# Kernel optimization log

Measured on AMD Instinct MI355X. Metric: run time of the kernel, lower is better.

Reference implementation:

```python
import jax, jax.numpy as jnp
import numpy as np

NUM_EMBEDDINGS = 1024
EMBEDDING_DIM = 256
COMMITMENT_COST = 0.25


def setup_inputs() -> dict:
    key = jax.random.key(0)
    k1, k2 = jax.random.split(key)
    z = jax.random.normal(k1, (64, EMBEDDING_DIM, 32, 32), dtype=jnp.float32)
    # torch init: uniform(-1/K, 1/K)
    emb = jax.random.uniform(k2, (NUM_EMBEDDINGS, EMBEDDING_DIM), dtype=jnp.float32,
                             minval=-1.0 / NUM_EMBEDDINGS, maxval=1.0 / NUM_EMBEDDINGS)
    return {"z": z, "emb": emb}


def reference(z, emb):
    B, D, H, W = z.shape
    # [B, H, W, D] -> [N, D]
    z_flat = jnp.transpose(z, (0, 2, 3, 1)).reshape(-1, D)
    # squared-euclidean distances to codebook: [N, K]
    d = ((z_flat * z_flat).sum(axis=1, keepdims=True)
         + (emb * emb).sum(axis=1)
         - 2.0 * z_flat @ emb.T)
    indices = jnp.argmin(d, axis=1)                      # [N]
    z_q = emb[indices].reshape(B, H, W, D).transpose(0, 3, 1, 2)  # [B, D, H, W]

    codebook_loss = jnp.mean((z_q - jax.lax.stop_gradient(z)) ** 2)
    commitment_loss = jnp.mean((z - jax.lax.stop_gradient(z_q)) ** 2)
    loss = codebook_loss + COMMITMENT_COST * commitment_loss

    # straight-through estimator
    z_q_out = z + jax.lax.stop_gradient(z_q - z)
    return z_q_out, loss, indices.reshape(B, H, W)
```

## Files before the change

### kernel.cpp

```cpp
#include <hip/hip_runtime.h>


typedef _Float16 f16x8 __attribute__((ext_vector_type(8)));
typedef float f32x4 __attribute__((ext_vector_type(4)));

#define VQ_W 1.5e-3f
#define SCR_LDS_BYTES 35328
#define RES_LDS_BYTES 33792

__device__ __forceinline__ float sq_rnd(float v) {
  float y = v * v;
  asm volatile("" : "+v"(y));
  return y;
}

__device__ float np_pw256_sq(const float* base, int stride) {
  float tot0, tot1;
  {
    const float* a = base;
    float r[8];
    #pragma unroll
    for (int j = 0; j < 8; ++j) r[j] = sq_rnd(a[j * stride]);
    #pragma unroll 1
    for (int i = 8; i < 128; i += 8) {
      #pragma unroll
      for (int j = 0; j < 8; ++j) r[j] += sq_rnd(a[(i + j) * stride]);
    }
    tot0 = ((r[0] + r[1]) + (r[2] + r[3])) + ((r[4] + r[5]) + (r[6] + r[7]));
  }
  {
    const float* a = base + 128 * stride;
    float r[8];
    #pragma unroll
    for (int j = 0; j < 8; ++j) r[j] = sq_rnd(a[j * stride]);
    #pragma unroll 1
    for (int i = 8; i < 128; i += 8) {
      #pragma unroll
      for (int j = 0; j < 8; ++j) r[j] += sq_rnd(a[(i + j) * stride]);
    }
    tot1 = ((r[0] + r[1]) + (r[2] + r[3])) + ((r[4] + r[5]) + (r[6] + r[7]));
  }
  return tot0 + tot1;
}

__global__ __launch_bounds__(256) void vq_pre(const float* __restrict__ emb,
                                              const float* __restrict__ z,
                                              _Float16* __restrict__ Ef,
                                              float* __restrict__ embT,
                                              float* __restrict__ e2,
                                              float* __restrict__ z2) {
  __shared__ float sm[256];
  const int tid = threadIdx.x;
  if (blockIdx.x < 1024) {
    const int g = blockIdx.x * 256 + tid;
    const float v = emb[g];
    Ef[g] = (_Float16)v;
    const int k = g >> 8, d = g & 255;
    embT[d * 1024 + k] = v;
    if (g < 1024) e2[g] = np_pw256_sq(emb + g * 256, 1);
    return;
  }
  const int blk = blockIdx.x - 1024;
  const int p = tid & 15;
  const int c = tid >> 4;
  const int n0 = blk * 16;
  const int n = n0 + p;
  const int bb = n >> 10, hw = n & 1023;
  const float* zp = z + bb * 262144 + hw;
  const int dbase = (c >> 3) * 128 + (c & 7);
  float r = sq_rnd(zp[dbase * 1024]);
  #pragma unroll
  for (int i = 1; i < 16; ++i) r += sq_rnd(zp[(dbase + 8 * i) * 1024]);
  sm[c * 16 + p] = r;
  __syncthreads();
  if (tid < 16) {
    const int pp = tid;
    float h0[8], h1[8];
    #pragma unroll
    for (int j = 0; j < 8; ++j) {
      h0[j] = sm[j * 16 + pp];
      h1[j] = sm[(8 + j) * 16 + pp];
    }
    const float tot0 = ((h0[0] + h0[1]) + (h0[2] + h0[3])) +
                       ((h0[4] + h0[5]) + (h0[6] + h0[7]));
    const float tot1 = ((h1[0] + h1[1]) + (h1[2] + h1[3])) +
                       ((h1[4] + h1[5]) + (h1[6] + h1[7]));
    z2[n0 + pp] = tot0 + tot1;
  }
}

__global__ __launch_bounds__(256, 4) void vq_screen(
    const float* __restrict__ z, const _Float16* __restrict__ Ef,
    const float* __restrict__ e2, const float* __restrict__ z2,
    int* __restrict__ gcnt, unsigned short* __restrict__ gcand) {
  extern __shared__ __align__(16) char smem[];
  unsigned* runminU = (unsigned*)(smem + 32768);
  int* cnt = (int*)(smem + 33024);
  unsigned short* cand = (unsigned short*)(smem + 33280);

  const int tid = threadIdx.x;
  const int blk = blockIdx.x;
  const int n0 = blk * 64;
  const int bb = blk >> 4;
  const int hw0 = (blk & 15) * 64;
  const float* zb = z + bb * 262144 + hw0;

  if (tid < 64) { runminU[tid] = 0x7F800000u; cnt[tid] = 0; }

  {
    const int p = tid & 63, dh = tid >> 6;
    #pragma unroll
    for (int dq = 0; dq < 8; ++dq) {
      const int d0 = dh * 64 + dq * 8;
      f16x8 hv;
      #pragma unroll
      for (int j = 0; j < 8; ++j) hv[j] = (_Float16)zb[(d0 + j) * 1024 + p];
      *(f16x8*)&smem[p * 512 + ((d0 * 2) ^ ((p & 7) * 16))] = hv;
    }
  }

  const int l = tid & 63;
  const int ln = l & 15;
  const int q = l >> 4;
  const int wc = tid >> 6;
  const int xr = (l & 7) * 16;

  float z2r[4][4];
  #pragma unroll
  for (int fi = 0; fi < 4; ++fi)
    #pragma unroll
    for (int rg = 0; rg < 4; ++rg)
      z2r[fi][rg] = z2[n0 + fi * 16 + q * 4 + rg];

  f32x4 acc[4][4];
  #pragma unroll
  for (int fi = 0; fi < 4; ++fi)
    #pragma unroll
    for (int fj = 0; fj < 4; ++fj) acc[fi][fj] = (f32x4){0.f, 0.f, 0.f, 0.f};

  __syncthreads();

  for (int cc = 0; cc < 4; ++cc) {
    const _Float16* Ebase = Ef + (cc * 256 + wc * 64 + ln) * 256 + q * 8;
    f16x8 bFb[2][4];
    #pragma unroll
    for (int fj = 0; fj < 4; ++fj)
      bFb[0][fj] = *(const f16x8*)(Ebase + fj * 16 * 256);
    #pragma unroll
    for (int ph = 0; ph < 8; ++ph) {
      const int cur = ph & 1, nxt = cur ^ 1;
      if (ph < 7) {
        #pragma unroll
        for (int fj = 0; fj < 4; ++fj)
          bFb[nxt][fj] = *(const f16x8*)(Ebase + fj * 16 * 256 + (ph + 1) * 32);
      }
      f16x8 aF[4];
      const int ab = (ph * 64 + q * 16) ^ xr;
      #pragma unroll
      for (int fi = 0; fi < 4; ++fi)
        aF[fi] = *(const f16x8*)&smem[(fi * 16 + ln) * 512 + ab];
      #pragma unroll
      for (int fi = 0; fi < 4; ++fi)
        #pragma unroll
        for (int fj = 0; fj < 4; ++fj)
          acc[fi][fj] = __builtin_amdgcn_mfma_f32_16x16x32_f16(
              aF[fi], bFb[cur][fj], acc[fi][fj], 0, 0, 0);
    }
    {
      const int cbase = cc * 256 + wc * 64 + ln;
      float e2v[4];
      #pragma unroll
      for (int fj = 0; fj < 4; ++fj) e2v[fj] = e2[cbase + fj * 16];
      #pragma unroll
      for (int fi = 0; fi < 4; ++fi) {
        #pragma unroll
        for (int rg = 0; rg < 4; ++rg) {
          float rm = 3.4e38f;
          #pragma unroll
          for (int fj = 0; fj < 4; ++fj)
            rm = fminf(rm, fmaf(-2.f, acc[fi][fj][rg], z2r[fi][rg] + e2v[fj]));
          rm = fminf(rm, __shfl_xor(rm, 1));
          rm = fminf(rm, __shfl_xor(rm, 2));
          rm = fminf(rm, __shfl_xor(rm, 4));
          rm = fminf(rm, __shfl_xor(rm, 8));
          if (ln == 0)
            atomicMin(&runminU[fi * 16 + q * 4 + rg], __float_as_uint(rm));
        }
      }
      __syncthreads();
      #pragma unroll
      for (int fi = 0; fi < 4; ++fi) {
        #pragma unroll
        for (int rg = 0; rg < 4; ++rg) {
          const int row = fi * 16 + q * 4 + rg;
          const float thr = __uint_as_float(runminU[row]) + VQ_W;
          #pragma unroll
          for (int fj = 0; fj < 4; ++fj) {
            const float sv = fmaf(-2.f, acc[fi][fj][rg], z2r[fi][rg] + e2v[fj]);
            if (sv <= thr) {
              const int slot = atomicAdd(&cnt[row], 1);
              if (slot < 16)
                cand[row * 16 + slot] = (unsigned short)(cbase + fj * 16);
            }
          }
        }
        #pragma unroll
        for (int fj = 0; fj < 4; ++fj) acc[fi][fj] = (f32x4){0.f, 0.f, 0.f, 0.f};
      }
    }
  }

  __syncthreads();
  if (tid < 64) gcnt[n0 + tid] = cnt[tid];
  {
    const int rr = tid >> 2, si = (tid & 3) * 4;
    *(uint2*)&gcand[(n0 + rr) * 16 + si] = *(const uint2*)&cand[rr * 16 + si];
  }
}

__global__ __launch_bounds__(256, 4) void vq_rescore(
    const float* __restrict__ z, const float* __restrict__ emb,
    const float* __restrict__ e2, const float* __restrict__ z2,
    const int* __restrict__ gcnt, const unsigned short* __restrict__ gcand,
    int* __restrict__ widx, float* __restrict__ out) {
  extern __shared__ __align__(16) char psmem[];
  float* zt = (float*)psmem;
  int* wid = (int*)(psmem + 33408);
  unsigned long long* best = (unsigned long long*)(psmem + 33536);

  const int tid = threadIdx.x;
  const int pg = tid & 7;
  const int ds = tid >> 3;
  const int w8 = tid >> 5;
  const int l = tid & 31;
  const int n0 = blockIdx.x << 5;
  const int bb = n0 >> 10, hw0 = n0 & 1023;
  const int n = n0 + l;

  const int c = gcnt[n];
  const bool need = __any(c >= 2);

  if (!need) {
    if (tid < 32) {
      const int v = gcand[(n0 + tid) * 16];
      widx[n0 + tid] = v;
      out[16777217 + n0 + tid] = (float)v;
    }
    return;
  }

  {
    const float* zb = z + bb * 262144 + hw0 + pg * 4;
    float4 zS[8];
    #pragma unroll
    for (int jj = 0; jj < 8; ++jj) zS[jj] = *(const float4*)&zb[(ds * 8 + jj) * 1024];
    #pragma unroll
    for (int jj = 0; jj < 8; ++jj) {
      const int d = ds * 8 + jj;
      zt[(pg * 4 + 0) * 257 + d] = zS[jj].x;
      zt[(pg * 4 + 1) * 257 + d] = zS[jj].y;
      zt[(pg * 4 + 2) * 257 + d] = zS[jj].z;
      zt[(pg * 4 + 3) * 257 + d] = zS[jj].w;
    }
  }
  if (tid < 32) best[tid] = ~0ULL;
  __syncthreads();

  if (c >= 2) {
    const float z2n = z2[n];
    const float* zrow = &zt[l * 257];
    if (c <= 16) {
      for (int s = w8; s < c; s += 8) {
        const int k = gcand[n * 16 + s];
        const float4* ep4 = (const float4*)(emb + k * 256);
        float a = 0.f;
        #pragma unroll 8
        for (int d4 = 0; d4 < 64; ++d4) {
          const float4 ev = ep4[d4];
          a = fmaf(zrow[d4 * 4 + 0], ev.x, a);
          a = fmaf(zrow[d4 * 4 + 1], ev.y, a);
          a = fmaf(zrow[d4 * 4 + 2], ev.z, a);
          a = fmaf(zrow[d4 * 4 + 3], ev.w, a);
        }
        const float sv = fmaf(-2.f, a, z2n + e2[k]);
        const unsigned long long key =
            ((unsigned long long)__float_as_uint(sv) << 10) | (unsigned)k;
        atomicMin(&best[l], key);
      }
    } else {
      for (int k = w8; k < 1024; k += 8) {
        const float4* ep4 = (const float4*)(emb + k * 256);
        float a = 0.f;
        #pragma unroll 8
        for (int d4 = 0; d4 < 64; ++d4) {
          const float4 ev = ep4[d4];
          a = fmaf(zrow[d4 * 4 + 0], ev.x, a);
          a = fmaf(zrow[d4 * 4 + 1], ev.y, a);
          a = fmaf(zrow[d4 * 4 + 2], ev.z, a);
          a = fmaf(zrow[d4 * 4 + 3], ev.w, a);
        }
        const float sv = fmaf(-2.f, a, z2n + e2[k]);
        const unsigned long long key =
            ((unsigned long long)__float_as_uint(sv) << 10) | (unsigned)k;
        atomicMin(&best[l], key);
      }
    }
  }
  __syncthreads();
  if (tid < 32) {
    const int cc = gcnt[n0 + tid];
    const int v = (cc == 1) ? (int)gcand[(n0 + tid) * 16]
                            : (int)(best[tid] & 1023ULL);
    widx[n0 + tid] = v;
    out[16777217 + n0 + tid] = (float)v;
  }
}

__global__ __launch_bounds__(256) void vq_out2(
    const float* __restrict__ z, const float* __restrict__ embT,
    const int* __restrict__ widx, float* __restrict__ out,
    double* __restrict__ partial) {
  __shared__ __align__(16) float et[4 * 1024];
  __shared__ double wv[4];
  const int tid = threadIdx.x;
  const int bb = blockIdx.x >> 6;
  const int d0 = (blockIdx.x & 63) * 4;

  const int4 myi = *(const int4*)&widx[bb * 1024 + tid * 4];
  #pragma unroll
  for (int it = 0; it < 4; ++it)
    *(float4*)&et[it * 1024 + tid * 4] =
        *(const float4*)&embT[(d0 + it) * 1024 + tid * 4];

  const float* zb = z + bb * 262144 + d0 * 1024 + tid * 4;
  float* ob = out + bb * 262144 + d0 * 1024 + tid * 4;
  float4 zv[4];
  #pragma unroll
  for (int dr = 0; dr < 4; ++dr) zv[dr] = *(const float4*)&zb[dr * 1024];
  __syncthreads();

  double ls = 0.0;
  #pragma unroll
  for (int dr = 0; dr < 4; ++dr) {
    const float* etr = &et[dr * 1024];
    float4 qv;
    qv.x = etr[myi.x];
    qv.y = etr[myi.y];
    qv.z = etr[myi.z];
    qv.w = etr[myi.w];
    float dx = qv.x - zv[dr].x, dy = qv.y - zv[dr].y;
    float dz = qv.z - zv[dr].z, dw = qv.w - zv[dr].w;
    asm volatile("" : "+v"(dx), "+v"(dy), "+v"(dz), "+v"(dw));
    float4 ov;
    ov.x = zv[dr].x + dx; ov.y = zv[dr].y + dy;
    ov.z = zv[dr].z + dz; ov.w = zv[dr].w + dw;
    *(float4*)&ob[dr * 1024] = ov;
    ls += (double)dx * dx + (double)dy * dy + (double)dz * dz + (double)dw * dw;
  }
  #pragma unroll
  for (int off = 32; off > 0; off >>= 1) ls += __shfl_down(ls, off);
  if ((tid & 63) == 0) wv[tid >> 6] = ls;
  __syncthreads();
  if (tid == 0)
    partial[blockIdx.x] = ((wv[0] + wv[1]) + (wv[2] + wv[3]));
}

__global__ __launch_bounds__(256) void vq_fin(const double* __restrict__ partial,
                                              float* __restrict__ out) {
  __shared__ double sd[4];
  const int tid = threadIdx.x;
  double s = 0.0;
  #pragma unroll 4
  for (int i = tid; i < 4096; i += 256) s += partial[i];
  #pragma unroll
  for (int off = 32; off > 0; off >>= 1) s += __shfl_down(s, off);
  if ((tid & 63) == 0) sd[tid >> 6] = s;
  __syncthreads();
  if (tid == 0)
    out[16777216] =
        (float)(1.25 * ((sd[0] + sd[1]) + (sd[2] + sd[3])) * (1.0 / 16777216.0));
}

extern "C" void kernel_launch(void* const* d_in, const int* in_sizes, int n_in,
                              void* d_out, int out_size, void* d_ws, size_t ws_size,
                              hipStream_t stream) {
  const float* z = (const float*)d_in[0];
  const float* emb = (const float*)d_in[1];
  float* out = (float*)d_out;
  char* ws = (char*)d_ws;
  int* widx = (int*)(ws + 64);
  float* e2 = (float*)(ws + 262208);
  float* z2 = (float*)(ws + 266304);
  int* gcnt = (int*)(ws + 528448);
  unsigned short* gcand = (unsigned short*)(ws + 790592);
  _Float16* Ef = (_Float16*)(ws + 2887744);
  float* embT = (float*)(ws + 3412032);
  double* partial = (double*)(ws + 4460608);

  hipFuncSetAttribute(reinterpret_cast<const void*>(vq_screen),
                      hipFuncAttributeMaxDynamicSharedMemorySize, SCR_LDS_BYTES);
  hipFuncSetAttribute(reinterpret_cast<const void*>(vq_rescore),
                      hipFuncAttributeMaxDynamicSharedMemorySize, RES_LDS_BYTES);

  vq_pre<<<5120, 256, 0, stream>>>(emb, z, Ef, embT, e2, z2);
  vq_screen<<<1024, 256, SCR_LDS_BYTES, stream>>>(z, Ef, e2, z2, gcnt, gcand);
  vq_rescore<<<2048, 256, RES_LDS_BYTES, stream>>>(z, emb, e2, z2, gcnt, gcand,
                                                   widx, out);
  vq_out2<<<4096, 256, 0, stream>>>(z, embT, widx, out, partial);
  vq_fin<<<1, 256, 0, stream>>>(partial, out);
}
```

Measured before the change: 205.0 us.

## Fuse z squared-norm computation into screening kernel's z tile load

Removes the separate z-norm pass from the preprocessing kernel and computes per-row squared norms inside vq_screen while converting z to fp16 in LDS. The second half of each row's sum is recomputed by re-reading z, chaining partial sums through LDS to preserve the original summation order. This eliminates a full extra read of z and many pre-kernel blocks, at the cost of extra LDS, extra barriers and some repeated global reads in the screen kernel.

```diff
diff --git a/kernel.cpp b/kernel.cpp
--- a/kernel.cpp
+++ b/kernel.cpp
@@ -5,7 +5,7 @@
 typedef float f32x4 __attribute__((ext_vector_type(4)));
 
 #define VQ_W 1.5e-3f
-#define SCR_LDS_BYTES 35328
+#define SCR_LDS_BYTES 40192
 #define RES_LDS_BYTES 33792
 
 __device__ __forceinline__ float sq_rnd(float v) {
@@ -44,59 +44,29 @@
 }
 
 __global__ __launch_bounds__(256) void vq_pre(const float* __restrict__ emb,
-                                              const float* __restrict__ z,
                                               _Float16* __restrict__ Ef,
                                               float* __restrict__ embT,
-                                              float* __restrict__ e2,
-                                              float* __restrict__ z2) {
-  __shared__ float sm[256];
+                                              float* __restrict__ e2) {
   const int tid = threadIdx.x;
-  if (blockIdx.x < 1024) {
-    const int g = blockIdx.x * 256 + tid;
-    const float v = emb[g];
-    Ef[g] = (_Float16)v;
-    const int k = g >> 8, d = g & 255;
-    embT[d * 1024 + k] = v;
-    if (g < 1024) e2[g] = np_pw256_sq(emb + g * 256, 1);
-    return;
-  }
-  const int blk = blockIdx.x - 1024;
-  const int p = tid & 15;
-  const int c = tid >> 4;
-  const int n0 = blk * 16;
-  const int n = n0 + p;
-  const int bb = n >> 10, hw = n & 1023;
-  const float* zp = z + bb * 262144 + hw;
-  const int dbase = (c >> 3) * 128 + (c & 7);
-  float r = sq_rnd(zp[dbase * 1024]);
-  #pragma unroll
-  for (int i = 1; i < 16; ++i) r += sq_rnd(zp[(dbase + 8 * i) * 1024]);
-  sm[c * 16 + p] = r;
-  __syncthreads();
-  if (tid < 16) {
-    const int pp = tid;
-    float h0[8], h1[8];
-    #pragma unroll
-    for (int j = 0; j < 8; ++j) {
-      h0[j] = sm[j * 16 + pp];
-      h1[j] = sm[(8 + j) * 16 + pp];
-    }
-    const float tot0 = ((h0[0] + h0[1]) + (h0[2] + h0[3])) +
-                       ((h0[4] + h0[5]) + (h0[6] + h0[7]));
-    const float tot1 = ((h1[0] + h1[1]) + (h1[2] + h1[3])) +
-                       ((h1[4] + h1[5]) + (h1[6] + h1[7]));
-    z2[n0 + pp] = tot0 + tot1;
-  }
+  const int g = blockIdx.x * 256 + tid;
+  const float v = emb[g];
+  Ef[g] = (_Float16)v;
+  const int k = g >> 8, d = g & 255;
+  embT[d * 1024 + k] = v;
+  if (g < 1024) e2[g] = np_pw256_sq(emb + g * 256, 1);
 }
 
 __global__ __launch_bounds__(256, 4) void vq_screen(
     const float* __restrict__ z, const _Float16* __restrict__ Ef,
-    const float* __restrict__ e2, const float* __restrict__ z2,
+    const float* __restrict__ e2, float* __restrict__ z2g,
     int* __restrict__ gcnt, unsigned short* __restrict__ gcand) {
   extern __shared__ __align__(16) char smem[];
   unsigned* runminU = (unsigned*)(smem + 32768);
   int* cnt = (int*)(smem + 33024);
   unsigned short* cand = (unsigned short*)(smem + 33280);
+  float* relay = (float*)(smem + 35328);
+  float* relay2 = (float*)(smem + 39424);
+  float* z2s = (float*)(smem + 39936);
 
   const int tid = threadIdx.x;
   const int blk = blockIdx.x;
@@ -107,17 +77,51 @@
 
   if (tid < 64) { runminU[tid] = 0x7F800000u; cnt[tid] = 0; }
 
+  const int p = tid & 63, dh = tid >> 6;
   {
-    const int p = tid & 63, dh = tid >> 6;
+    float r[8];
+    #pragma unroll
+    for (int j = 0; j < 8; ++j) r[j] = 0.f;
     #pragma unroll
     for (int dq = 0; dq < 8; ++dq) {
       const int d0 = dh * 64 + dq * 8;
       f16x8 hv;
       #pragma unroll
-      for (int j = 0; j < 8; ++j) hv[j] = (_Float16)zb[(d0 + j) * 1024 + p];
+      for (int j = 0; j < 8; ++j) {
+        const float x = zb[(d0 + j) * 1024 + p];
+        r[j] += sq_rnd(x);
+        hv[j] = (_Float16)x;
+      }
       *(f16x8*)&smem[p * 512 + ((d0 * 2) ^ ((p & 7) * 16))] = hv;
     }
-  }
+    if (!(dh & 1)) {
+      const int h = dh >> 1;
+      #pragma unroll
+      for (int j = 0; j < 8; ++j) relay[p * 16 + h * 8 + j] = r[j];
+    }
+  }
+  __syncthreads();
+  if (dh & 1) {
+    const int h = dh >> 1;
+    float rr[8];
+    #pragma unroll
+    for (int j = 0; j < 8; ++j) rr[j] = relay[p * 16 + h * 8 + j];
+    #pragma unroll
+    for (int dq = 0; dq < 8; ++dq) {
+      const int d0 = dh * 64 + dq * 8;
+      #pragma unroll
+      for (int j = 0; j < 8; ++j) rr[j] += sq_rnd(zb[(d0 + j) * 1024 + p]);
+    }
+    relay2[p * 2 + h] = ((rr[0] + rr[1]) + (rr[2] + rr[3])) +
+                        ((rr[4] + rr[5]) + (rr[6] + rr[7]));
+  }
+  __syncthreads();
+  if (tid < 64) {
+    const float zz = relay2[tid * 2] + relay2[tid * 2 + 1];
+    z2s[tid] = zz;
+    z2g[n0 + tid] = zz;
+  }
+  __syncthreads();
 
   const int l = tid & 63;
   const int ln = l & 15;
@@ -130,15 +134,13 @@
   for (int fi = 0; fi < 4; ++fi)
     #pragma unroll
     for (int rg = 0; rg < 4; ++rg)
-      z2r[fi][rg] = z2[n0 + fi * 16 + q * 4 + rg];
+      z2r[fi][rg] = z2s[fi * 16 + q * 4 + rg];
 
   f32x4 acc[4][4];
   #pragma unroll
   for (int fi = 0; fi < 4; ++fi)
     #pragma unroll
     for (int fj = 0; fj < 4; ++fj) acc[fi][fj] = (f32x4){0.f, 0.f, 0.f, 0.f};
-
-  __syncthreads();
 
   for (int cc = 0; cc < 4; ++cc) {
     const _Float16* Ebase = Ef + (cc * 256 + wc * 64 + ln) * 256 + q * 8;
@@ -227,6 +229,7 @@
   float* zt = (float*)psmem;
   int* wid = (int*)(psmem + 33408);
   unsigned long long* best = (unsigned long long*)(psmem + 33536);
+  (void)wid;
 
   const int tid = threadIdx.x;
   const int pg = tid & 7;
@@ -402,7 +405,7 @@
   hipFuncSetAttribute(reinterpret_cast<const void*>(vq_rescore),
                       hipFuncAttributeMaxDynamicSharedMemorySize, RES_LDS_BYTES);
 
-  vq_pre<<<5120, 256, 0, stream>>>(emb, z, Ef, embT, e2, z2);
+  vq_pre<<<1024, 256, 0, stream>>>(emb, Ef, embT, e2);
   vq_screen<<<1024, 256, SCR_LDS_BYTES, stream>>>(z, Ef, e2, z2, gcnt, gcand);
   vq_rescore<<<2048, 256, RES_LDS_BYTES, stream>>>(z, emb, e2, z2, gcnt, gcand,
                                                    widx, out);
```

After: 217.0 us. 5.9% more time.
